# Performance work log

Hardware: AMD Instinct MI355X
Metric: run time of the kernel (lower is better)

Reference implementation:

```python
import jax, jax.numpy as jnp
import numpy as np

N_STATE = 12
HID = 128
BS = 16384


def setup_inputs() -> dict:
    key = jax.random.key(0)
    ks = jax.random.split(key, 16)
    s = 0.05
    inp = {
        'state': jax.random.normal(ks[0], (BS, N_STATE), dtype=jnp.float32),
        'safe_m': jax.random.uniform(ks[1], (N_STATE,), minval=0.5, maxval=2.0, dtype=jnp.float32),
        'safe_l': -jax.random.uniform(ks[2], (N_STATE,), minval=0.5, maxval=2.0, dtype=jnp.float32),
        'W0': jax.random.normal(ks[3], (HID, N_STATE), dtype=jnp.float32) * s,
        'b0': jax.random.normal(ks[4], (HID,), dtype=jnp.float32) * s,
        'W1': jax.random.normal(ks[5], (HID, HID), dtype=jnp.float32) * s,
        'b1': jax.random.normal(ks[6], (HID,), dtype=jnp.float32) * s,
        'W2': jax.random.normal(ks[7], (HID, HID), dtype=jnp.float32) * s,
        'b2': jax.random.normal(ks[8], (HID,), dtype=jnp.float32) * s,
        'W3': jax.random.normal(ks[9], (HID, HID), dtype=jnp.float32) * s,
        'b3': jax.random.normal(ks[10], (HID,), dtype=jnp.float32) * s,
        'Wout': jax.random.normal(ks[11], (1, HID), dtype=jnp.float32) * s,
        'bout': jax.random.normal(ks[12], (1,), dtype=jnp.float32) * s,
    }
    return inp


def _linear(V, JV, W, b):
    # V: (bs, in) -> (bs, out); JV: (bs, in, n) -> (bs, out, n)
    return V @ W.T + b, jnp.einsum('oh,bhn->bon', W, JV)


def _tanh(V, JV):
    V = jnp.tanh(V)
    # diag_embed(1 - V^2) @ JV  ==  elementwise row scaling
    return V, (1.0 - V * V)[:, :, None] * JV


def reference(state, safe_m, safe_l, W0, b0, W1, b1, W2, b2, W3, b3, Wout, bout):
    bs = state.shape[0]
    x_center = (safe_m + safe_l) * 0.5            # (n,)
    x_range = (safe_m - safe_l) * 0.5             # (n,)
    x_norm = (state - x_center) / x_range         # (bs, n)

    # JV initialized to diag(1/x_range), broadcast over batch
    JV = jnp.broadcast_to(jnp.diag(1.0 / x_range), (bs, N_STATE, N_STATE))

    V, JV = _linear(x_norm, JV, W0, b0)   # input_linear
    V, JV = _tanh(V, JV)                  # input_activation
    V, JV = _linear(V, JV, W1, b1)        # layer_0_linear
    V, JV = _tanh(V, JV)                  # layer_0_activation
    V, JV = _linear(V, JV, W2, b2)        # layer_1_linear
    V, JV = _tanh(V, JV)                  # layer_1_activation
    V, JV = _linear(V, JV, W3, b3)        # layer_2_linear (no activation)
    V, JV = _linear(V, JV, Wout, bout)    # output_linear -> V:(bs,1), JV:(bs,1,n)

    # HJH = hstack(h, Jh) generalized over batch: (bs, 1 + n_state)
    return jnp.concatenate([V, JV[:, 0, :]], axis=1)
```

## Files before the change

kernel.cpp:

```cpp
#include <hip/hip_runtime.h>

#define NS  12
#define HID 128
#define SPB 8
#define RB  128

typedef __attribute__((ext_vector_type(8))) short bf8_t;
typedef __attribute__((ext_vector_type(4))) float f4_t;

#define O_W0H 0
#define O_W0L 2048
#define O_WH(i) (4096 + (i) * 16384)
#define O_WL(i) (O_WH(i) + 8192)

__device__ __forceinline__ unsigned f2bf_u(float f) {
  unsigned u = __float_as_uint(f);
  return (u + 0x7FFFu + ((u >> 16) & 1u)) >> 16;
}
__device__ __forceinline__ float bf2f(unsigned h) { return __uint_as_float(h << 16); }

__device__ __forceinline__ unsigned cvtpk(float a, float b) {
  unsigned r;
  asm("v_cvt_pk_bf16_f32 %0, %1, %2" : "=v"(r) : "v"(a), "v"(b));
  return r;
}
__device__ __forceinline__ float fast_tanh(float v) {
  float vc = fminf(fmaxf(v, -15.f), 15.f);
  float e = __expf(vc + vc);
  return (e - 1.f) * __builtin_amdgcn_rcpf(e + 1.f);
}
__device__ __forceinline__ f4_t mfma16(bf8_t a, bf8_t b, f4_t c) {
  return __builtin_amdgcn_mfma_f32_16x16x32_bf16(a, b, c, 0, 0, 0);
}

__global__ __launch_bounds__(256) void prep_w(
    const float* __restrict__ W0, const float* __restrict__ W1,
    const float* __restrict__ W2, const float* __restrict__ W3,
    unsigned* __restrict__ ws)
{
  int t = blockIdx.x * 256 + threadIdx.x;
  if (t >= 53248) return;
  int tile = t >> 9;
  int pos  = t & 511;
  int g = pos >> 7, o = (pos >> 3) & 15, j = pos & 7;

  const float* src; int kdim; unsigned hoff, loff; int lt;
  if (tile < 8) { src = W0; kdim = NS; hoff = O_W0H; loff = O_W0L; lt = tile; }
  else {
    int li = (tile - 8) >> 5;  lt = (tile - 8) & 31;
    src = (li == 0) ? W1 : (li == 1) ? W2 : W3;
    kdim = HID; hoff = O_WH(li); loff = O_WL(li);
  }
  int ks = (tile < 8) ? 0 : (lt >> 3);
  int mt = (tile < 8) ? lt : (lt & 7);
  int k = ks * 32 + g * 8 + j;
  int orow = mt * 16 + o;
  float v = (k < kdim) ? src[orow * kdim + k] : 0.f;
  unsigned h = f2bf_u(v);
  unsigned lo = f2bf_u(v - bf2f(h));
  int idx = lt * 512 + pos;
  ((unsigned short*)(ws + hoff))[idx] = (unsigned short)h;
  ((unsigned short*)(ws + loff))[idx] = (unsigned short)lo;
}

template<int KSUBS, bool ACT>
__device__ __forceinline__ void layer(
    unsigned* __restrict__ S, const unsigned* __restrict__ whi,
    const unsigned* __restrict__ wlo, const float* __restrict__ bias,
    int lane, int l15, int g, int bp, int rwave, int mwave, int mt0)
{
  f4_t acc[4][2];
  #pragma unroll
  for (int a = 0; a < 4; ++a)
    #pragma unroll
    for (int b = 0; b < 2; ++b) acc[a][b] = (f4_t){0.f, 0.f, 0.f, 0.f};

  const int aswz = (l15 & 7) << 2;
  #pragma unroll
  for (int ks = 0; ks < KSUBS; ++ks) {
    bf8_t bh[2], bl[2];
    #pragma unroll
    for (int mm = 0; mm < 2; ++mm) {
      int tb = (ks * 8 + mt0 + mm) * 256 + lane * 4;
      bh[mm] = __builtin_bit_cast(bf8_t, *(const uint4*)(whi + tb));
      bl[mm] = __builtin_bit_cast(bf8_t, *(const uint4*)(wlo + tb));
    }
    #pragma unroll
    for (int rs = 0; rs < 4; ++rs) {
      int row = rwave + rs * 16 + l15;
      int idx = row * 64 + ((ks * 16 + g * 4) ^ aswz);
      bf8_t avh = __builtin_bit_cast(bf8_t, *(const uint4*)(S + idx));
      bf8_t avl = __builtin_bit_cast(bf8_t, *(const uint4*)(S + 8192 + idx));
      #pragma unroll
      for (int mm = 0; mm < 2; ++mm) {
        acc[rs][mm] = mfma16(avh, bh[mm], acc[rs][mm]);
        acc[rs][mm] = mfma16(avh, bl[mm], acc[rs][mm]);
        acc[rs][mm] = mfma16(avl, bh[mm], acc[rs][mm]);
      }
    }
  }
  __syncthreads();

  const bool even = (lane & 1) == 0;
  #pragma unroll
  for (int rs = 0; rs < 4; ++rs) {
    #pragma unroll
    for (int mm = 0; mm < 2; ++mm) {
      int col = mwave + mm * 16 + l15;
      float bv = bias[col];
      f4_t a = acc[rs][mm];
      int rb = rwave + rs * 16 + g * 4;
      if (ACT) {
        float vb = __int_as_float(__builtin_amdgcn_ds_bpermute(bp, __float_as_int(a[0])));
        float t = fast_tanh(vb + bv);
        float s = 1.f - t * t;
        a[0] = (g == 0) ? t : a[0] * s;
        a[1] *= s; a[2] *= s; a[3] *= s;
        int wc = col >> 1;
        #pragma unroll
        for (int j = 0; j < 4; ++j) {
          float pv = __shfl_xor(a[j], 1);
          float vlo = even ? a[j] : pv;
          float vhi = even ? pv : a[j];
          unsigned wh = cvtpk(vlo, vhi);
          float rl = vlo - __uint_as_float(wh << 16);
          float rh = vhi - __uint_as_float(wh & 0xFFFF0000u);
          unsigned wl = cvtpk(rl, rh);
          if (even == (j < 2)) {
            int row = rb + j;
            int idx = row * 64 + (wc ^ ((row & 7) << 2));
            S[idx] = wh;
            S[8192 + idx] = wl;
          }
        }
      } else {
        if (g == 0) a[0] += bv;
        float* Xf = (float*)S;
        #pragma unroll
        for (int j = 0; j < 4; ++j) {
          int row = rb + j;
          Xf[row * 128 + (col ^ ((row & 7) << 2))] = a[j];
        }
      }
    }
  }
  __syncthreads();
}

__global__ __launch_bounds__(512, 4) void mlp_jac(
    const float* __restrict__ state,
    const float* __restrict__ safe_m, const float* __restrict__ safe_l,
    const unsigned* __restrict__ ws,
    const float* __restrict__ b0, const float* __restrict__ b1,
    const float* __restrict__ b2, const float* __restrict__ b3,
    const float* __restrict__ Wout, const float* __restrict__ bout,
    float* __restrict__ out, int bs)
{
  __shared__ unsigned S[16384];
  __shared__ float red[512];

  const int tid  = threadIdx.x;
  const int lane = tid & 63;
  const int wid  = tid >> 6;
  const int widR = wid >> 2;
  const int widN = wid & 3;
  const int rwave = widR * 64;
  const int mwave = widN * 32;
  const int mt0   = widN * 2;
  const int l15 = lane & 15;
  const int g   = lane >> 4;
  const int bp  = l15 * 4;
  const int s0  = blockIdx.x * SPB;

  for (int i = tid; i < RB * 16; i += 512) {
    int r = i >> 4, kp = i & 15;
    int b = r >> 4, rr = r & 15;
    int sidx = s0 + b;
    float v[2];
    #pragma unroll
    for (int t = 0; t < 2; ++t) {
      int k = kp * 2 + t;
      float val = 0.f;
      if (k < NS) {
        float m = safe_m[k], l = safe_l[k];
        float inv = 2.f / (m - l);
        if (rr == 0) {
          float sv = (sidx < bs) ? state[sidx * NS + k] : 0.f;
          val = (sv - 0.5f * (m + l)) * inv;
        } else if (k == rr - 1) val = inv;
      }
      v[t] = val;
    }
    unsigned wh = cvtpk(v[0], v[1]);
    float rl = v[0] - __uint_as_float(wh << 16);
    float rh = v[1] - __uint_as_float(wh & 0xFFFF0000u);
    unsigned wl = cvtpk(rl, rh);
    int idx = r * 64 + (kp ^ ((r & 7) << 2));
    S[idx] = wh;
    S[8192 + idx] = wl;
  }
  __syncthreads();

  layer<1, true >(S, ws + O_W0H,  ws + O_W0L,  b0, lane, l15, g, bp, rwave, mwave, mt0);
  layer<4, true >(S, ws + O_WH(0), ws + O_WL(0), b1, lane, l15, g, bp, rwave, mwave, mt0);
  layer<4, true >(S, ws + O_WH(1), ws + O_WL(1), b2, lane, l15, g, bp, rwave, mwave, mt0);
  layer<4, false>(S, ws + O_WH(2), ws + O_WL(2), b3, lane, l15, g, bp, rwave, mwave, mt0);

  {
    const float* Xf = (const float*)S;
    int r = tid & 127;
    int q = tid >> 7;
    float a = 0.f;
    #pragma unroll
    for (int kk = 0; kk < 8; ++kk) {
      int c = q * 32 + kk * 4;
      float4 x = *(const float4*)(Xf + r * 128 + (c ^ ((r & 7) << 2)));
      a = fmaf(Wout[c + 0], x.x, a);
      a = fmaf(Wout[c + 1], x.y, a);
      a = fmaf(Wout[c + 2], x.z, a);
      a = fmaf(Wout[c + 3], x.w, a);
    }
    red[tid] = a;
  }
  __syncthreads();
  if (tid < 128) {
    float tot = red[tid] + red[tid + 128] + red[tid + 256] + red[tid + 384];
    int b = tid >> 4, rr = tid & 15;
    int sidx = s0 + b;
    if (sidx < bs && rr < 13) {
      if (rr == 0) tot += bout[0];
      out[sidx * 13 + rr] = tot;
    }
  }
}

extern "C" void kernel_launch(void* const* d_in, const int* in_sizes, int n_in,
                              void* d_out, int out_size, void* d_ws, size_t ws_size,
                              hipStream_t stream)
{
  const float* state  = (const float*)d_in[0];
  const float* safe_m = (const float*)d_in[1];
  const float* safe_l = (const float*)d_in[2];
  const float* W0   = (const float*)d_in[3];
  const float* b0   = (const float*)d_in[4];
  const float* W1   = (const float*)d_in[5];
  const float* b1   = (const float*)d_in[6];
  const float* W2   = (const float*)d_in[7];
  const float* b2   = (const float*)d_in[8];
  const float* W3   = (const float*)d_in[9];
  const float* b3   = (const float*)d_in[10];
  const float* Wout = (const float*)d_in[11];
  const float* bout = (const float*)d_in[12];
  unsigned* ws = (unsigned*)d_ws;
  float* out = (float*)d_out;

  const int bs = in_sizes[0] / NS;

  prep_w<<<(53248 + 255) / 256, 256, 0, stream>>>(W0, W1, W2, W3, ws);

  const int nblocks = (bs + SPB - 1) / SPB;
  mlp_jac<<<nblocks, 512, 0, stream>>>(state, safe_m, safe_l, ws,
      b0, b1, b2, b3, Wout, bout, out, bs);
}
```

Measured before the change: 178.0 us.

## Prefetch weight fragments, streamline epilogue shuffles, and pack weight prep stores

```diff
diff --git a/kernel.cpp b/kernel.cpp
--- a/kernel.cpp
+++ b/kernel.cpp
@@ -24,11 +24,6 @@
   asm("v_cvt_pk_bf16_f32 %0, %1, %2" : "=v"(r) : "v"(a), "v"(b));
   return r;
 }
-__device__ __forceinline__ float fast_tanh(float v) {
-  float vc = fminf(fmaxf(v, -15.f), 15.f);
-  float e = __expf(vc + vc);
-  return (e - 1.f) * __builtin_amdgcn_rcpf(e + 1.f);
-}
 __device__ __forceinline__ f4_t mfma16(bf8_t a, bf8_t b, f4_t c) {
   return __builtin_amdgcn_mfma_f32_16x16x32_bf16(a, b, c, 0, 0, 0);
 }
@@ -39,9 +34,9 @@
     unsigned* __restrict__ ws)
 {
   int t = blockIdx.x * 256 + threadIdx.x;
-  if (t >= 53248) return;
-  int tile = t >> 9;
-  int pos  = t & 511;
+  if (t >= 26624) return;
+  int tile = t >> 8;
+  int pos  = (t & 255) * 2;
   int g = pos >> 7, o = (pos >> 3) & 15, j = pos & 7;
 
   const float* src; int kdim; unsigned hoff, loff; int lt;
@@ -53,14 +48,15 @@
   }
   int ks = (tile < 8) ? 0 : (lt >> 3);
   int mt = (tile < 8) ? lt : (lt & 7);
-  int k = ks * 32 + g * 8 + j;
+  int k0 = ks * 32 + g * 8 + j;
   int orow = mt * 16 + o;
-  float v = (k < kdim) ? src[orow * kdim + k] : 0.f;
-  unsigned h = f2bf_u(v);
-  unsigned lo = f2bf_u(v - bf2f(h));
-  int idx = lt * 512 + pos;
-  ((unsigned short*)(ws + hoff))[idx] = (unsigned short)h;
-  ((unsigned short*)(ws + loff))[idx] = (unsigned short)lo;
+  float v0 = (k0 < kdim)     ? src[orow * kdim + k0]     : 0.f;
+  float v1 = (k0 + 1 < kdim) ? src[orow * kdim + k0 + 1] : 0.f;
+  unsigned h0 = f2bf_u(v0), h1 = f2bf_u(v1);
+  unsigned l0 = f2bf_u(v0 - bf2f(h0)), l1 = f2bf_u(v1 - bf2f(h1));
+  int widx = (lt * 512 + pos) >> 1;
+  (ws + hoff)[widx] = h0 | (h1 << 16);
+  (ws + loff)[widx] = l0 | (l1 << 16);
 }
 
 template<int KSUBS, bool ACT>
@@ -76,14 +72,25 @@
     for (int b = 0; b < 2; ++b) acc[a][b] = (f4_t){0.f, 0.f, 0.f, 0.f};
 
   const int aswz = (l15 & 7) << 2;
+
+  bf8_t bh[2][2], bl[2][2];
+  #pragma unroll
+  for (int mm = 0; mm < 2; ++mm) {
+    int tb = (mt0 + mm) * 256 + lane * 4;
+    bh[0][mm] = __builtin_bit_cast(bf8_t, *(const uint4*)(whi + tb));
+    bl[0][mm] = __builtin_bit_cast(bf8_t, *(const uint4*)(wlo + tb));
+  }
+
   #pragma unroll
   for (int ks = 0; ks < KSUBS; ++ks) {
-    bf8_t bh[2], bl[2];
-    #pragma unroll
-    for (int mm = 0; mm < 2; ++mm) {
-      int tb = (ks * 8 + mt0 + mm) * 256 + lane * 4;
-      bh[mm] = __builtin_bit_cast(bf8_t, *(const uint4*)(whi + tb));
-      bl[mm] = __builtin_bit_cast(bf8_t, *(const uint4*)(wlo + tb));
+    const int cur = ks & 1, nxt = cur ^ 1;
+    if (ks + 1 < KSUBS) {
+      #pragma unroll
+      for (int mm = 0; mm < 2; ++mm) {
+        int tb = ((ks + 1) * 8 + mt0 + mm) * 256 + lane * 4;
+        bh[nxt][mm] = __builtin_bit_cast(bf8_t, *(const uint4*)(whi + tb));
+        bl[nxt][mm] = __builtin_bit_cast(bf8_t, *(const uint4*)(wlo + tb));
+      }
     }
     #pragma unroll
     for (int rs = 0; rs < 4; ++rs) {
@@ -93,54 +100,70 @@
       bf8_t avl = __builtin_bit_cast(bf8_t, *(const uint4*)(S + 8192 + idx));
       #pragma unroll
       for (int mm = 0; mm < 2; ++mm) {
-        acc[rs][mm] = mfma16(avh, bh[mm], acc[rs][mm]);
-        acc[rs][mm] = mfma16(avh, bl[mm], acc[rs][mm]);
-        acc[rs][mm] = mfma16(avl, bh[mm], acc[rs][mm]);
-      }
-    }
-  }
-  __syncthreads();
-
-  const bool even = (lane & 1) == 0;
+        acc[rs][mm] = mfma16(avh, bh[cur][mm], acc[rs][mm]);
+        acc[rs][mm] = mfma16(avh, bl[cur][mm], acc[rs][mm]);
+        acc[rs][mm] = mfma16(avl, bh[cur][mm], acc[rs][mm]);
+      }
+    }
+  }
+
+  float bv[2];
+  #pragma unroll
+  for (int mm = 0; mm < 2; ++mm) bv[mm] = bias[mwave + mm * 16 + l15];
+
+  __syncthreads();
+
+  const bool ev = (lane & 1) == 0;
   #pragma unroll
   for (int rs = 0; rs < 4; ++rs) {
+    int rb = rwave + rs * 16 + g * 4;
+    int row0 = rb + (ev ? 0 : 2);
+    int row1 = row0 + 1;
+    int a0b = row0 * 64, sw0 = (row0 & 7) << 2;
+    int a1b = row1 * 64, sw1 = (row1 & 7) << 2;
     #pragma unroll
     for (int mm = 0; mm < 2; ++mm) {
       int col = mwave + mm * 16 + l15;
-      float bv = bias[col];
       f4_t a = acc[rs][mm];
-      int rb = rwave + rs * 16 + g * 4;
       if (ACT) {
-        float vb = __int_as_float(__builtin_amdgcn_ds_bpermute(bp, __float_as_int(a[0])));
-        float t = fast_tanh(vb + bv);
-        float s = 1.f - t * t;
+        float pre = a[0] + bv[mm];
+        float vb = __int_as_float(__builtin_amdgcn_ds_bpermute(bp, __float_as_int(pre)));
+        float e = __expf(fminf(vb, 15.f) * 2.f);
+        float r = __builtin_amdgcn_rcpf(e + 1.f);
+        float t = (e - 1.f) * r;
+        float s = fmaf(-t, t, 1.f);
         a[0] = (g == 0) ? t : a[0] * s;
         a[1] *= s; a[2] *= s; a[3] *= s;
-        int wc = col >> 1;
-        #pragma unroll
-        for (int j = 0; j < 4; ++j) {
-          float pv = __shfl_xor(a[j], 1);
-          float vlo = even ? a[j] : pv;
-          float vhi = even ? pv : a[j];
-          unsigned wh = cvtpk(vlo, vhi);
-          float rl = vlo - __uint_as_float(wh << 16);
-          float rh = vhi - __uint_as_float(wh & 0xFFFF0000u);
-          unsigned wl = cvtpk(rl, rh);
-          if (even == (j < 2)) {
-            int row = rb + j;
-            int idx = row * 64 + (wc ^ ((row & 7) << 2));
-            S[idx] = wh;
-            S[8192 + idx] = wl;
-          }
-        }
       } else {
-        if (g == 0) a[0] += bv;
+        if (g == 0) a[0] += bv[mm];
+      }
+      float p0 = __shfl_xor(a[0], 1);
+      float p1 = __shfl_xor(a[1], 1);
+      float p2 = __shfl_xor(a[2], 1);
+      float p3 = __shfl_xor(a[3], 1);
+      float u0 = ev ? a[0] : p2;
+      float u1 = ev ? p0 : a[2];
+      float v0 = ev ? a[1] : p3;
+      float v1 = ev ? p1 : a[3];
+      if (ACT) {
+        int wc = (mwave + mm * 16) / 2 + (l15 >> 1);
+        unsigned wh0 = cvtpk(u0, u1);
+        float rl0 = u0 - __uint_as_float(wh0 << 16);
+        float rh0 = u1 - __uint_as_float(wh0 & 0xFFFF0000u);
+        unsigned wl0 = cvtpk(rl0, rh0);
+        unsigned wh1 = cvtpk(v0, v1);
+        float rl1 = v0 - __uint_as_float(wh1 << 16);
+        float rh1 = v1 - __uint_as_float(wh1 & 0xFFFF0000u);
+        unsigned wl1 = cvtpk(rl1, rh1);
+        int i0 = a0b + (wc ^ sw0);
+        int i1 = a1b + (wc ^ sw1);
+        S[i0] = wh0;  S[8192 + i0] = wl0;
+        S[i1] = wh1;  S[8192 + i1] = wl1;
+      } else {
         float* Xf = (float*)S;
-        #pragma unroll
-        for (int j = 0; j < 4; ++j) {
-          int row = rb + j;
-          Xf[row * 128 + (col ^ ((row & 7) << 2))] = a[j];
-        }
+        int ceven = (mwave + mm * 16) + (l15 & ~1);
+        *(float2*)(Xf + row0 * 128 + (ceven ^ sw0)) = make_float2(u0, u1);
+        *(float2*)(Xf + row1 * 128 + (ceven ^ sw1)) = make_float2(v0, v1);
       }
     }
   }
@@ -256,7 +279,7 @@
 
   const int bs = in_sizes[0] / NS;
 
-  prep_w<<<(53248 + 255) / 256, 256, 0, stream>>>(W0, W1, W2, W3, ws);
+  prep_w<<<104, 256, 0, stream>>>(W0, W1, W2, W3, ws);
 
   const int nblocks = (bs + SPB - 1) / SPB;
   mlp_jac<<<nblocks, 512, 0, stream>>>(state, safe_m, safe_l, ws,
```

Result: faster. 167.9 us (-5.7%).
